# Optimization experiments

Measured on AMD Instinct MI355X. Metric: run time of the kernel, lower is better.

Reference implementation:

```python
import jax, jax.numpy as jnp
import numpy as np

EMBED = 1024
HEADS = 16
HEAD_DIM = EMBED // HEADS
LN_EPS = 1e-5


def _layer_norm(x, g, b):
    m = jnp.mean(x, axis=-1, keepdims=True)
    v = jnp.mean((x - m) ** 2, axis=-1, keepdims=True)
    return (x - m) / jnp.sqrt(v + LN_EPS) * g + b


def _rope(x):
    # x: (b, H, n, D); standard rotary: freqs repeated (cat(freqs, freqs)), rotate_half
    D = x.shape[-1]
    n = x.shape[2]
    inv_freq = 1.0 / (10000.0 ** (jnp.arange(0, D, 2, dtype=jnp.float32) / D))
    freqs = jnp.arange(n, dtype=jnp.float32)[:, None] * inv_freq[None, :]  # (n, D/2)
    emb = jnp.concatenate([freqs, freqs], axis=-1)  # (n, D)
    cos, sin = jnp.cos(emb), jnp.sin(emb)
    rot = jnp.concatenate([-x[..., D // 2:], x[..., : D // 2]], axis=-1)
    return x * cos + rot * sin


def setup_inputs() -> dict:
    key = jax.random.key(0)
    ks = jax.random.split(key, 8)
    E = EMBED
    s_in = 1.0 / np.sqrt(E)
    return {
        "x": jax.random.normal(ks[0], (2, 2048, E), dtype=jnp.float32),
        "in_proj_w": jax.random.uniform(ks[1], (3 * E, E), jnp.float32, -s_in, s_in),
        "in_proj_b": jnp.zeros((3 * E,), jnp.float32),
        "out_proj_w": jax.random.uniform(ks[2], (E, E), jnp.float32, -s_in, s_in),
        "out_proj_b": jnp.zeros((E,), jnp.float32),
        "geglu_w": jax.random.uniform(ks[3], (2 * E, E), jnp.float32, -s_in, s_in),
        "geglu_b": jnp.zeros((2 * E,), jnp.float32),
        "ln1_g": jnp.ones((E,), jnp.float32),
        "ln1_b": jnp.zeros((E,), jnp.float32),
        "ln2_g": jnp.ones((E,), jnp.float32),
        "ln2_b": jnp.zeros((E,), jnp.float32),
    }


def reference(x, in_proj_w, in_proj_b, out_proj_w, out_proj_b,
              geglu_w, geglu_b, ln1_g, ln1_b, ln2_g, ln2_b):
    b, n, E = x.shape
    H, D = HEADS, HEAD_DIM

    # RoPE applied to raw x (q = k = v = x in the module)
    xh = x.reshape(b, n, H, D).transpose(0, 2, 1, 3)  # (b,H,n,D)
    qr = _rope(xh)
    kr = qr  # q and k are identical pre-projection
    q = qr.transpose(0, 2, 1, 3).reshape(b, n, E)
    k = kr.transpose(0, 2, 1, 3).reshape(b, n, E)
    v = x

    # MultiheadAttention (batch-first semantics): in-proj, per-head SDPA, out-proj
    w_q, w_k, w_v = jnp.split(in_proj_w, 3, axis=0)
    b_q, b_k, b_v = jnp.split(in_proj_b, 3, axis=0)
    qp = (q @ w_q.T + b_q).reshape(b, n, H, D).transpose(0, 2, 1, 3)
    kp = (k @ w_k.T + b_k).reshape(b, n, H, D).transpose(0, 2, 1, 3)
    vp = (v @ w_v.T + b_v).reshape(b, n, H, D).transpose(0, 2, 1, 3)
    scores = jnp.einsum("bhqd,bhkd->bhqk", qp, kp) / jnp.sqrt(jnp.float32(D))
    attn = jax.nn.softmax(scores, axis=-1)
    ctx = jnp.einsum("bhqk,bhkd->bhqd", attn, vp)
    ctx = ctx.transpose(0, 2, 1, 3).reshape(b, n, E)
    attn_out = ctx @ out_proj_w.T + out_proj_b

    # residual + LN1
    h = _layer_norm(x + attn_out, ln1_g, ln1_b)

    # GeGLU: Linear(E -> 2E), chunk, value * gelu(gate) (exact erf gelu like torch)
    proj = h @ geglu_w.T + geglu_b
    val, gate = jnp.split(proj, 2, axis=-1)
    fc_out = val * jax.nn.gelu(gate, approximate=False)

    # residual + LN2
    return _layer_norm(h + fc_out, ln2_g, ln2_b)
```

## Files before the change

kernel.cpp:

```cpp
#include <hip/hip_runtime.h>


typedef __bf16 bf16;
typedef bf16 bf16x8 __attribute__((ext_vector_type(8)));
typedef bf16 bf16x4 __attribute__((ext_vector_type(4)));
typedef float f32x4 __attribute__((ext_vector_type(4)));
typedef float f32x16 __attribute__((ext_vector_type(16)));

#define EMB 1024
#define SEQ 2048
#define NTOK 4096
#define NH 16
#define HD 64

__device__ __forceinline__ f32x4 mfma16(bf16x8 a, bf16x8 b, f32x4 c) {
  return __builtin_amdgcn_mfma_f32_16x16x32_bf16(a, b, c, 0, 0, 0);
}
__device__ __forceinline__ f32x16 mfma32(bf16x8 a, bf16x8 b, f32x16 c) {
  return __builtin_amdgcn_mfma_f32_32x32x16_bf16(a, b, c, 0, 0, 0);
}

__device__ __forceinline__ void gll16(const void* g, void* l) {
  __builtin_amdgcn_global_load_lds(
      (const __attribute__((address_space(1))) void*)g,
      (__attribute__((address_space(3))) void*)l, 16, 0, 0);
}

__device__ __forceinline__ unsigned pk2(float a, float b) {
  union { bf16 h[2]; unsigned u; } t;
  t.h[0] = (bf16)a; t.h[1] = (bf16)b;
  return t.u;
}


__global__ __launch_bounds__(256) void rope_cast(
    const float* __restrict__ x, bf16* __restrict__ xb, bf16* __restrict__ qr) {
  int idx = blockIdx.x * 256 + threadIdx.x;
  int row = idx >> 9;
  int i = idx & 511;
  int h = i >> 5, d2 = i & 31;
  int pos = row & (SEQ - 1);
  int c0 = h * HD + d2;
  size_t base = (size_t)row * EMB;
  float x0 = x[base + c0], x1 = x[base + c0 + 32];
  float invf = exp2f(-(float)d2 * 0.4152410118609203f);
  float ang = (float)pos * invf;
  float sn, cs;
  sincosf(ang, &sn, &cs);
  qr[base + c0] = (bf16)(x0 * cs - x1 * sn);
  qr[base + c0 + 32] = (bf16)(x1 * cs + x0 * sn);
  xb[base + c0] = (bf16)x0;
  xb[base + c0 + 32] = (bf16)x1;
}

__global__ __launch_bounds__(256) void cast_w(
    const float* __restrict__ w, bf16* __restrict__ o, int n) {
  int i = (blockIdx.x * 256 + threadIdx.x) * 4;
  if (i < n) {
    float4 f = *(const float4*)(w + i);
    o[i] = (bf16)f.x; o[i + 1] = (bf16)f.y;
    o[i + 2] = (bf16)f.z; o[i + 3] = (bf16)f.w;
  }
}

__global__ __launch_bounds__(256) void gemm_in(
    const bf16* __restrict__ Aq, const bf16* __restrict__ Ax,
    const bf16* __restrict__ W, const float* __restrict__ bias,
    bf16* __restrict__ qk, bf16* __restrict__ vT) {
  __shared__ bf16 As[128 * 32];
  __shared__ bf16 Bs[128 * 32];
  const int tid = threadIdx.x, lane = tid & 63, wave = tid >> 6;
  const int quad = lane >> 4, l16 = lane & 15;
  const int m0 = blockIdx.y * 128, n0 = blockIdx.x * 128;
  const bf16* A = (n0 < 2048) ? Aq : Ax;
  const int K = 1024;
  const int wm = (wave >> 1) * 64, wn = (wave & 1) * 64;
  const int srow = wave * 32 + (lane >> 2);
  const int scol = (lane & 3) * 8;
  f32x4 acc[4][4] = {};
  for (int k0 = 0; k0 < K; k0 += 32) {
    __syncthreads();
    gll16(A + (size_t)(m0 + srow) * K + k0 + scol, As + wave * 1024);
    gll16(A + (size_t)(m0 + srow + 16) * K + k0 + scol, As + wave * 1024 + 512);
    gll16(W + (size_t)(n0 + srow) * K + k0 + scol, Bs + wave * 1024);
    gll16(W + (size_t)(n0 + srow + 16) * K + k0 + scol, Bs + wave * 1024 + 512);
    __syncthreads();
    bf16x8 af[4], bw[4];
#pragma unroll
    for (int t = 0; t < 4; ++t) {
      af[t] = *(const bf16x8*)(As + (wm + t * 16 + l16) * 32 + quad * 8);
      bw[t] = *(const bf16x8*)(Bs + (wn + t * 16 + l16) * 32 + quad * 8);
    }
#pragma unroll
    for (int mt = 0; mt < 4; ++mt)
#pragma unroll
      for (int nt = 0; nt < 4; ++nt)
        acc[mt][nt] = mfma16(af[mt], bw[nt], acc[mt][nt]);
  }
  if (n0 < 2048) {
#pragma unroll
    for (int mt = 0; mt < 4; ++mt)
      for (int nt = 0; nt < 4; ++nt) {
        const int n = n0 + wn + nt * 16 + l16;
        const float bv = bias[n];
#pragma unroll
        for (int r = 0; r < 4; ++r) {
          const int m = m0 + wm + mt * 16 + quad * 4 + r;
          qk[(size_t)m * 2048 + n] = (bf16)(acc[mt][nt][r] + bv);
        }
      }
  } else {
#pragma unroll
    for (int mt = 0; mt < 4; ++mt)
      for (int nt = 0; nt < 4; ++nt) {
        const int n = n0 + wn + nt * 16 + l16;
        const float bv = bias[n];
        const int m = m0 + wm + mt * 16 + quad * 4;
        const int bb = m >> 11, s = m & 2047;
        bf16x4 pkv;
#pragma unroll
        for (int r = 0; r < 4; ++r) pkv[r] = (bf16)(acc[mt][nt][r] + bv);
        *(bf16x4*)(vT + (((size_t)bb * 1024 + (n - 2048)) << 11) + s) = pkv;
      }
  }
}

__global__ __launch_bounds__(256) void gemm_bt(
    const bf16* __restrict__ A, const bf16* __restrict__ W,
    const float* __restrict__ bias,
    float* __restrict__ outF, bf16* __restrict__ outB,
    int M, int N, int K) {
  __shared__ bf16 As[128 * 32];
  __shared__ bf16 Bs[128 * 32];
  const int tid = threadIdx.x, lane = tid & 63, wave = tid >> 6;
  const int quad = lane >> 4, l16 = lane & 15;
  const int m0 = blockIdx.y * 128, n0 = blockIdx.x * 128;
  const int wm = (wave >> 1) * 64, wn = (wave & 1) * 64;
  const int srow = wave * 32 + (lane >> 2);
  const int scol = (lane & 3) * 8;
  f32x4 acc[4][4] = {};
  for (int k0 = 0; k0 < K; k0 += 32) {
    __syncthreads();
    gll16(A + (size_t)(m0 + srow) * K + k0 + scol, As + wave * 1024);
    gll16(A + (size_t)(m0 + srow + 16) * K + k0 + scol, As + wave * 1024 + 512);
    gll16(W + (size_t)(n0 + srow) * K + k0 + scol, Bs + wave * 1024);
    gll16(W + (size_t)(n0 + srow + 16) * K + k0 + scol, Bs + wave * 1024 + 512);
    __syncthreads();
    bf16x8 af[4], bw[4];
#pragma unroll
    for (int t = 0; t < 4; ++t) {
      af[t] = *(const bf16x8*)(As + (wm + t * 16 + l16) * 32 + quad * 8);
      bw[t] = *(const bf16x8*)(Bs + (wn + t * 16 + l16) * 32 + quad * 8);
    }
#pragma unroll
    for (int mt = 0; mt < 4; ++mt)
#pragma unroll
      for (int nt = 0; nt < 4; ++nt)
        acc[mt][nt] = mfma16(af[mt], bw[nt], acc[mt][nt]);
  }
#pragma unroll
  for (int mt = 0; mt < 4; ++mt)
    for (int nt = 0; nt < 4; ++nt) {
      const int n = n0 + wn + nt * 16 + l16;
      const float bv = bias ? bias[n] : 0.0f;
#pragma unroll
      for (int r = 0; r < 4; ++r) {
        const int m = m0 + wm + mt * 16 + quad * 4 + r;
        const float v = acc[mt][nt][r] + bv;
        if (outF) outF[(size_t)m * N + n] = v;
        if (outB) outB[(size_t)m * N + n] = (bf16)v;
      }
    }
}

__global__ __launch_bounds__(256) void gemm_bt64(
    const bf16* __restrict__ A, const bf16* __restrict__ W,
    const float* __restrict__ bias, float* __restrict__ outF,
    int M, int N, int K) {
  __shared__ bf16 As[128 * 32];
  __shared__ bf16 Bs[64 * 32];
  const int tid = threadIdx.x, lane = tid & 63, wave = tid >> 6;
  const int quad = lane >> 4, l16 = lane & 15;
  const int m0 = blockIdx.y * 128, n0 = blockIdx.x * 64;
  const int wm = (wave >> 1) * 64, wn = (wave & 1) * 32;
  const int srow = wave * 32 + (lane >> 2);
  const int srowB = wave * 16 + (lane >> 2);
  const int scol = (lane & 3) * 8;
  f32x4 acc[4][2] = {};
  for (int k0 = 0; k0 < K; k0 += 32) {
    __syncthreads();
    gll16(A + (size_t)(m0 + srow) * K + k0 + scol, As + wave * 1024);
    gll16(A + (size_t)(m0 + srow + 16) * K + k0 + scol, As + wave * 1024 + 512);
    gll16(W + (size_t)(n0 + srowB) * K + k0 + scol, Bs + wave * 512);
    __syncthreads();
    bf16x8 af[4], bw[2];
#pragma unroll
    for (int t = 0; t < 4; ++t)
      af[t] = *(const bf16x8*)(As + (wm + t * 16 + l16) * 32 + quad * 8);
#pragma unroll
    for (int t = 0; t < 2; ++t)
      bw[t] = *(const bf16x8*)(Bs + (wn + t * 16 + l16) * 32 + quad * 8);
#pragma unroll
    for (int mt = 0; mt < 4; ++mt)
#pragma unroll
      for (int nt = 0; nt < 2; ++nt)
        acc[mt][nt] = mfma16(af[mt], bw[nt], acc[mt][nt]);
  }
#pragma unroll
  for (int mt = 0; mt < 4; ++mt)
    for (int nt = 0; nt < 2; ++nt) {
      const int n = n0 + wn + nt * 16 + l16;
      const float bv = bias[n];
#pragma unroll
      for (int r = 0; r < 4; ++r) {
        const int m = m0 + wm + mt * 16 + quad * 4 + r;
        outF[(size_t)m * N + n] = acc[mt][nt][r] + bv;
      }
    }
}

__global__ __launch_bounds__(256) void attn7(
    const bf16* __restrict__ QK, const bf16* __restrict__ VT,
    bf16* __restrict__ ctx) {
  __shared__ __align__(16) bf16 Ks[2][64 * 64];
  __shared__ __align__(16) bf16 Vs[2][64 * 64];
  __shared__ float Linv[4][32];
  const int tid = threadIdx.x, lane = tid & 63, wave = tid >> 6;
  const int hi = lane >> 5, l31 = lane & 31, l7 = lane & 7;
  const int bid = blockIdx.x;
  const int hb = (bid & 7) * 4 + ((bid >> 3) & 3);
  const int qt = bid >> 5;
  const int h = hb & 15, b = hb >> 4;

  bf16x8 qf[4];
  {
    const int qrow = qt * 128 + wave * 32 + l31;
    const bf16* qp = QK + (size_t)(b * SEQ + qrow) * 2048 + h * HD + hi * 8;
#pragma unroll
    for (int t = 0; t < 4; ++t) {
      bf16x8 v = *(const bf16x8*)(qp + t * 16);
#pragma unroll
      for (int j = 0; j < 8; ++j) v[j] = (bf16)((float)v[j] * 0.125f);
      qf[t] = v;
    }
  }
  f32x16 o0 = {}, o1 = {};
  float lpart = 0.0f;

  const int srow = tid >> 3;
  const int sc16 = tid & 7;
  const bf16* kg = QK + (size_t)(b * SEQ) * 2048 + 1024 + h * HD + sc16 * 8;
  const bf16* vg = VT + ((size_t)(b * NH + h) * HD) * 2048 + sc16 * 8;
  const int g4lo = 2 * sc16 - (sc16 & 1);

  bf16x8 kcur[2], vcur[2];
#pragma unroll
  for (int p = 0; p < 2; ++p) {
    const int row = p * 32 + srow;
    kcur[p] = *(const bf16x8*)(kg + (size_t)row * 2048);
    vcur[p] = *(const bf16x8*)(vg + (size_t)row * 2048);
  }
#pragma unroll
  for (int p = 0; p < 2; ++p) {
    const int row = p * 32 + srow;
    const int m2 = (row & 7) << 1;
    *(bf16x8*)(Ks[0] + row * 64 + ((sc16 ^ (row & 7)) * 8)) = kcur[p];
    union { bf16x8 v; unsigned long long q[2]; } u2;
    u2.v = vcur[p];
    *(unsigned long long*)(Vs[0] + row * 64 + ((g4lo ^ m2) * 4)) = u2.q[0];
    *(unsigned long long*)(Vs[0] + row * 64 + (((g4lo + 2) ^ m2) * 4)) = u2.q[1];
  }
#pragma unroll
  for (int p = 0; p < 2; ++p) {
    const int row = p * 32 + srow;
    kcur[p] = *(const bf16x8*)(kg + (size_t)(64 + row) * 2048);
    vcur[p] = *(const bf16x8*)(vg + (size_t)row * 2048 + 64);
  }

  for (int t = 0; t < 32; ++t) {
    __syncthreads();
    const bf16* ks = Ks[t & 1];
    const bf16* vs = Vs[t & 1];
    if (t + 1 < 32) {
      bf16* kd = Ks[(t + 1) & 1];
      bf16* vd = Vs[(t + 1) & 1];
#pragma unroll
      for (int p = 0; p < 2; ++p) {
        const int row = p * 32 + srow;
        const int m2 = (row & 7) << 1;
        *(bf16x8*)(kd + row * 64 + ((sc16 ^ (row & 7)) * 8)) = kcur[p];
        union { bf16x8 v; unsigned long long q[2]; } u2;
        u2.v = vcur[p];
        *(unsigned long long*)(vd + row * 64 + ((g4lo ^ m2) * 4)) = u2.q[0];
        *(unsigned long long*)(vd + row * 64 + (((g4lo + 2) ^ m2) * 4)) = u2.q[1];
      }
      if (t + 2 < 32) {
        const int kb2 = (t + 2) * 64;
#pragma unroll
        for (int p = 0; p < 2; ++p) {
          const int row = p * 32 + srow;
          kcur[p] = *(const bf16x8*)(kg + (size_t)(kb2 + row) * 2048);
          vcur[p] = *(const bf16x8*)(vg + (size_t)row * 2048 + kb2);
        }
      }
    }
    f32x16 s0 = {}, s1 = {};
#pragma unroll
    for (int tt = 0; tt < 4; ++tt) {
      const int swc = ((tt * 2 + hi) ^ l7) * 8;
      bf16x8 k0 = *(const bf16x8*)(ks + l31 * 64 + swc);
      bf16x8 k1 = *(const bf16x8*)(ks + (32 + l31) * 64 + swc);
      s0 = mfma32(k0, qf[tt], s0);
      s1 = mfma32(k1, qf[tt], s1);
    }
    unsigned u[16];
#pragma unroll
    for (int g = 0; g < 8; ++g) {
      const int base = (g & 3) * 4;
      float e0, e1, e2, e3;
      if (g < 4) {
        e0 = __expf(s0[base]); e1 = __expf(s0[base + 1]);
        e2 = __expf(s0[base + 2]); e3 = __expf(s0[base + 3]);
      } else {
        e0 = __expf(s1[base]); e1 = __expf(s1[base + 1]);
        e2 = __expf(s1[base + 2]); e3 = __expf(s1[base + 3]);
      }
      lpart += (e0 + e1) + (e2 + e3);
      u[g * 2] = pk2(e0, e1);
      u[g * 2 + 1] = pk2(e2, e3);
    }
#pragma unroll
    for (int kk = 0; kk < 4; ++kk) {
      union { unsigned w[4]; bf16x8 v; } fw;
      fw.w[0] = u[4 * kk]; fw.w[1] = u[4 * kk + 1];
      fw.w[2] = u[4 * kk + 2]; fw.w[3] = u[4 * kk + 3];
      const int swz = (4 * kk + 2 * hi) ^ (l7 << 1);
      bf16x8 v0 = *(const bf16x8*)(vs + l31 * 64 + swz * 4);
      bf16x8 v1 = *(const bf16x8*)(vs + (32 + l31) * 64 + swz * 4);
      o0 = mfma32(fw.v, v0, o0);
      o1 = mfma32(fw.v, v1, o1);
    }
  }
  float ltot = lpart + __shfl_xor(lpart, 32, 64);
  if (lane < 32) Linv[wave][lane] = 1.0f / ltot;
#pragma unroll
  for (int r = 0; r < 16; ++r) {
    const int qloc = (r & 3) + 8 * (r >> 2) + 4 * hi;
    const float inv = Linv[wave][qloc];
    const int qrow = qt * 128 + wave * 32 + qloc;
    bf16* cp = ctx + (size_t)(b * SEQ + qrow) * EMB + h * HD;
    cp[l31] = (bf16)(o0[r] * inv);
    cp[32 + l31] = (bf16)(o1[r] * inv);
  }
}

__global__ __launch_bounds__(256) void ln1_k(
    const float* __restrict__ x, const float* __restrict__ ao,
    const float* __restrict__ g, const float* __restrict__ bta,
    float* __restrict__ hF, bf16* __restrict__ hB) {
  int row = blockIdx.x, tid = threadIdx.x;
  const float* xr = x + (size_t)row * EMB;
  const float* ar = ao + (size_t)row * EMB;
  float v[4], s = 0.0f, s2 = 0.0f;
#pragma unroll
  for (int i = 0; i < 4; ++i) {
    float t = xr[tid + i * 256] + ar[tid + i * 256];
    v[i] = t; s += t; s2 += t * t;
  }
#pragma unroll
  for (int off = 1; off < 64; off <<= 1) {
    s += __shfl_xor(s, off, 64);
    s2 += __shfl_xor(s2, off, 64);
  }
  __shared__ float red[8];
  int wave = tid >> 6, lane = tid & 63;
  if (lane == 0) { red[wave] = s; red[4 + wave] = s2; }
  __syncthreads();
  s = red[0] + red[1] + red[2] + red[3];
  s2 = red[4] + red[5] + red[6] + red[7];
  float mean = s * (1.0f / EMB);
  float var = s2 * (1.0f / EMB) - mean * mean;
  float inv = rsqrtf(var + 1e-5f);
#pragma unroll
  for (int i = 0; i < 4; ++i) {
    int c = tid + i * 256;
    float t = (v[i] - mean) * inv * g[c] + bta[c];
    hF[(size_t)row * EMB + c] = t;
    hB[(size_t)row * EMB + c] = (bf16)t;
  }
}

__global__ __launch_bounds__(256) void geglu_ln2(
    const float* __restrict__ h, const bf16* __restrict__ proj,
    const float* __restrict__ g, const float* __restrict__ bta,
    float* __restrict__ out) {
  int row = blockIdx.x, tid = threadIdx.x;
  const float* hr = h + (size_t)row * EMB;
  const bf16* pr = proj + (size_t)row * 2048;
  float v[4], s = 0.0f, s2 = 0.0f;
#pragma unroll
  for (int i = 0; i < 4; ++i) {
    int c = tid + i * 256;
    float val = (float)pr[c];
    float gate = (float)pr[1024 + c];
    float ge = 0.5f * gate * (1.0f + erff(gate * 0.70710678f));
    float t = hr[c] + val * ge;
    v[i] = t; s += t; s2 += t * t;
  }
#pragma unroll
  for (int off = 1; off < 64; off <<= 1) {
    s += __shfl_xor(s, off, 64);
    s2 += __shfl_xor(s2, off, 64);
  }
  __shared__ float red[8];
  int wave = tid >> 6, lane = tid & 63;
  if (lane == 0) { red[wave] = s; red[4 + wave] = s2; }
  __syncthreads();
  s = red[0] + red[1] + red[2] + red[3];
  s2 = red[4] + red[5] + red[6] + red[7];
  float mean = s * (1.0f / EMB);
  float var = s2 * (1.0f / EMB) - mean * mean;
  float inv = rsqrtf(var + 1e-5f);
#pragma unroll
  for (int i = 0; i < 4; ++i) {
    int c = tid + i * 256;
    out[(size_t)row * EMB + c] = (v[i] - mean) * inv * g[c] + bta[c];
  }
}

extern "C" void kernel_launch(void* const* d_in, const int* in_sizes, int n_in,
                              void* d_out, int out_size, void* d_ws, size_t ws_size,
                              hipStream_t stream) {
  const float* x = (const float*)d_in[0];
  const float* inW = (const float*)d_in[1];
  const float* inB = (const float*)d_in[2];
  const float* outW = (const float*)d_in[3];
  const float* opB = (const float*)d_in[4];
  const float* ggW = (const float*)d_in[5];
  const float* ggB = (const float*)d_in[6];
  const float* g1 = (const float*)d_in[7];
  const float* b1 = (const float*)d_in[8];
  const float* g2 = (const float*)d_in[9];
  const float* b2 = (const float*)d_in[10];
  float* out = (float*)d_out;
  char* ws = (char*)d_ws;
  const size_t MB = 1ull << 20;
  bf16* xb = (bf16*)(ws);
  bf16* qr = (bf16*)(ws + 8 * MB);
  bf16* ctx = (bf16*)(ws + 8 * MB);
  bf16* wI = (bf16*)(ws + 16 * MB);
  bf16* wO = (bf16*)(ws + 22 * MB);
  bf16* wG = (bf16*)(ws + 24 * MB);
  bf16* qk = (bf16*)(ws + 28 * MB);
  bf16* projB = (bf16*)(ws + 28 * MB);
  bf16* vbT = (bf16*)(ws + 44 * MB);
  float* ao = (float*)(ws + 44 * MB);
  bf16* hB = (bf16*)(ws + 60 * MB);

  rope_cast<<<NTOK * 512 / 256, 256, 0, stream>>>(x, xb, qr);
  cast_w<<<(3072 * 1024 / 4) / 256, 256, 0, stream>>>(inW, wI, 3072 * 1024);
  cast_w<<<(1024 * 1024 / 4) / 256, 256, 0, stream>>>(outW, wO, 1024 * 1024);
  cast_w<<<(2048 * 1024 / 4) / 256, 256, 0, stream>>>(ggW, wG, 2048 * 1024);
  gemm_in<<<dim3(24, 32), 256, 0, stream>>>(qr, xb, wI, inB, qk, vbT);
  attn7<<<512, 256, 0, stream>>>(qk, vbT, ctx);
  gemm_bt64<<<dim3(16, 32), 256, 0, stream>>>(ctx, wO, opB, ao,
                                              NTOK, 1024, 1024);
  ln1_k<<<NTOK, 256, 0, stream>>>(x, ao, g1, b1, ao, hB);
  gemm_bt<<<dim3(16, 32), 256, 0, stream>>>(hB, wG, ggB, nullptr, projB,
                                            NTOK, 2048, 1024);
  geglu_ln2<<<NTOK, 256, 0, stream>>>(ao, projB, g2, b2, out);
}
```

Before: 273.8 us.

## Split attention keys across wave pairs and reduce partial outputs in LDS

The attention kernel now gives each block 64 query rows instead of 128, and each pair of waves splits every 64-key tile into two halves. Partial outputs and softmax denominators are combined through shared memory at the end, and the launch grid doubles to 1024 blocks. The V tile staging also changes to two 8-byte global loads per row followed by a single 16-byte swizzled LDS store. The aim is more parallelism and occupancy on the attention stage, at the cost of loading each K/V tile for half as many queries and adding an extra reduction and barriers.

New measurement: 282.0 us. 3.0% more time.

```diff
diff --git a/kernel.cpp b/kernel.cpp
--- a/kernel.cpp
+++ b/kernel.cpp
@@ -219,14 +219,15 @@
     }
 }
 
-__global__ __launch_bounds__(256) void attn7(
+__global__ __launch_bounds__(256) void attn8(
     const bf16* __restrict__ QK, const bf16* __restrict__ VT,
     bf16* __restrict__ ctx) {
-  __shared__ __align__(16) bf16 Ks[2][64 * 64];
-  __shared__ __align__(16) bf16 Vs[2][64 * 64];
-  __shared__ float Linv[4][32];
+  __shared__ __align__(16) bf16 Ks[2][4096];
+  __shared__ __align__(16) bf16 Vs[2][4096];
+  __shared__ float Linv2[2][32];
   const int tid = threadIdx.x, lane = tid & 63, wave = tid >> 6;
   const int hi = lane >> 5, l31 = lane & 31, l7 = lane & 7;
+  const int qgrp = wave & 1, khalf = wave >> 1;
   const int bid = blockIdx.x;
   const int hb = (bid & 7) * 4 + ((bid >> 3) & 3);
   const int qt = bid >> 5;
@@ -234,7 +235,7 @@
 
   bf16x8 qf[4];
   {
-    const int qrow = qt * 128 + wave * 32 + l31;
+    const int qrow = qt * 64 + qgrp * 32 + l31;
     const bf16* qp = QK + (size_t)(b * SEQ + qrow) * 2048 + h * HD + hi * 8;
 #pragma unroll
     for (int t = 0; t < 4; ++t) {
@@ -249,32 +250,35 @@
 
   const int srow = tid >> 3;
   const int sc16 = tid & 7;
+  const int tq = sc16 >> 1;
+  const int og = tq * 16 + (sc16 & 1) * 4;
   const bf16* kg = QK + (size_t)(b * SEQ) * 2048 + 1024 + h * HD + sc16 * 8;
-  const bf16* vg = VT + ((size_t)(b * NH + h) * HD) * 2048 + sc16 * 8;
-  const int g4lo = 2 * sc16 - (sc16 & 1);
-
-  bf16x8 kcur[2], vcur[2];
+  const bf16* vgr = VT + ((size_t)(b * NH + h) * HD) * 2048;
+
+  bf16x8 kcur[2];
+  uint2 va[2], vb[2];
 #pragma unroll
   for (int p = 0; p < 2; ++p) {
     const int row = p * 32 + srow;
     kcur[p] = *(const bf16x8*)(kg + (size_t)row * 2048);
-    vcur[p] = *(const bf16x8*)(vg + (size_t)row * 2048);
+    va[p] = *(const uint2*)(vgr + (size_t)row * 2048 + og);
+    vb[p] = *(const uint2*)(vgr + (size_t)row * 2048 + og + 8);
   }
 #pragma unroll
   for (int p = 0; p < 2; ++p) {
     const int row = p * 32 + srow;
-    const int m2 = (row & 7) << 1;
-    *(bf16x8*)(Ks[0] + row * 64 + ((sc16 ^ (row & 7)) * 8)) = kcur[p];
-    union { bf16x8 v; unsigned long long q[2]; } u2;
-    u2.v = vcur[p];
-    *(unsigned long long*)(Vs[0] + row * 64 + ((g4lo ^ m2) * 4)) = u2.q[0];
-    *(unsigned long long*)(Vs[0] + row * 64 + (((g4lo + 2) ^ m2) * 4)) = u2.q[1];
+    const int sw = row * 64 + ((sc16 ^ (row & 7)) * 8);
+    *(bf16x8*)(Ks[0] + sw) = kcur[p];
+    union { uint2 u2[2]; bf16x8 v; } vv;
+    vv.u2[0] = va[p]; vv.u2[1] = vb[p];
+    *(bf16x8*)(Vs[0] + sw) = vv.v;
   }
 #pragma unroll
   for (int p = 0; p < 2; ++p) {
     const int row = p * 32 + srow;
     kcur[p] = *(const bf16x8*)(kg + (size_t)(64 + row) * 2048);
-    vcur[p] = *(const bf16x8*)(vg + (size_t)row * 2048 + 64);
+    va[p] = *(const uint2*)(vgr + (size_t)row * 2048 + 64 + og);
+    vb[p] = *(const uint2*)(vgr + (size_t)row * 2048 + 64 + og + 8);
   }
 
   for (int t = 0; t < 32; ++t) {
@@ -287,12 +291,11 @@
 #pragma unroll
       for (int p = 0; p < 2; ++p) {
         const int row = p * 32 + srow;
-        const int m2 = (row & 7) << 1;
-        *(bf16x8*)(kd + row * 64 + ((sc16 ^ (row & 7)) * 8)) = kcur[p];
-        union { bf16x8 v; unsigned long long q[2]; } u2;
-        u2.v = vcur[p];
-        *(unsigned long long*)(vd + row * 64 + ((g4lo ^ m2) * 4)) = u2.q[0];
-        *(unsigned long long*)(vd + row * 64 + (((g4lo + 2) ^ m2) * 4)) = u2.q[1];
+        const int sw = row * 64 + ((sc16 ^ (row & 7)) * 8);
+        *(bf16x8*)(kd + sw) = kcur[p];
+        union { uint2 u2[2]; bf16x8 v; } vv;
+        vv.u2[0] = va[p]; vv.u2[1] = vb[p];
+        *(bf16x8*)(vd + sw) = vv.v;
       }
       if (t + 2 < 32) {
         const int kb2 = (t + 2) * 64;
@@ -300,40 +303,35 @@
         for (int p = 0; p < 2; ++p) {
           const int row = p * 32 + srow;
           kcur[p] = *(const bf16x8*)(kg + (size_t)(kb2 + row) * 2048);
-          vcur[p] = *(const bf16x8*)(vg + (size_t)row * 2048 + kb2);
+          va[p] = *(const uint2*)(vgr + (size_t)row * 2048 + kb2 + og);
+          vb[p] = *(const uint2*)(vgr + (size_t)row * 2048 + kb2 + og + 8);
         }
       }
     }
-    f32x16 s0 = {}, s1 = {};
+    f32x16 s0 = {};
 #pragma unroll
     for (int tt = 0; tt < 4; ++tt) {
-      const int swc = ((tt * 2 + hi) ^ l7) * 8;
-      bf16x8 k0 = *(const bf16x8*)(ks + l31 * 64 + swc);
-      bf16x8 k1 = *(const bf16x8*)(ks + (32 + l31) * 64 + swc);
-      s0 = mfma32(k0, qf[tt], s0);
-      s1 = mfma32(k1, qf[tt], s1);
-    }
-    unsigned u[16];
-#pragma unroll
-    for (int g = 0; g < 8; ++g) {
-      const int base = (g & 3) * 4;
-      float e0, e1, e2, e3;
-      if (g < 4) {
-        e0 = __expf(s0[base]); e1 = __expf(s0[base + 1]);
-        e2 = __expf(s0[base + 2]); e3 = __expf(s0[base + 3]);
-      } else {
-        e0 = __expf(s1[base]); e1 = __expf(s1[base + 1]);
-        e2 = __expf(s1[base + 2]); e3 = __expf(s1[base + 3]);
-      }
+      bf16x8 kf = *(const bf16x8*)(
+          ks + (khalf * 32 + l31) * 64 + (((tt * 2 + hi) ^ l7) * 8));
+      s0 = mfma32(kf, qf[tt], s0);
+    }
+    unsigned u[8];
+#pragma unroll
+    for (int g = 0; g < 4; ++g) {
+      float e0 = __expf(s0[g * 4]);
+      float e1 = __expf(s0[g * 4 + 1]);
+      float e2 = __expf(s0[g * 4 + 2]);
+      float e3 = __expf(s0[g * 4 + 3]);
       lpart += (e0 + e1) + (e2 + e3);
       u[g * 2] = pk2(e0, e1);
       u[g * 2 + 1] = pk2(e2, e3);
     }
 #pragma unroll
-    for (int kk = 0; kk < 4; ++kk) {
+    for (int kl = 0; kl < 2; ++kl) {
+      const int kk = 2 * khalf + kl;
       union { unsigned w[4]; bf16x8 v; } fw;
-      fw.w[0] = u[4 * kk]; fw.w[1] = u[4 * kk + 1];
-      fw.w[2] = u[4 * kk + 2]; fw.w[3] = u[4 * kk + 3];
+      fw.w[0] = u[4 * kl]; fw.w[1] = u[4 * kl + 1];
+      fw.w[2] = u[4 * kl + 2]; fw.w[3] = u[4 * kl + 3];
       const int swz = (4 * kk + 2 * hi) ^ (l7 << 1);
       bf16x8 v0 = *(const bf16x8*)(vs + l31 * 64 + swz * 4);
       bf16x8 v1 = *(const bf16x8*)(vs + (32 + l31) * 64 + swz * 4);
@@ -341,16 +339,45 @@
       o1 = mfma32(fw.v, v1, o1);
     }
   }
-  float ltot = lpart + __shfl_xor(lpart, 32, 64);
-  if (lane < 32) Linv[wave][lane] = 1.0f / ltot;
-#pragma unroll
-  for (int r = 0; r < 16; ++r) {
-    const int qloc = (r & 3) + 8 * (r >> 2) + 4 * hi;
-    const float inv = Linv[wave][qloc];
-    const int qrow = qt * 128 + wave * 32 + qloc;
-    bf16* cp = ctx + (size_t)(b * SEQ + qrow) * EMB + h * HD;
-    cp[l31] = (bf16)(o0[r] * inv);
-    cp[32 + l31] = (bf16)(o1[r] * inv);
+  __syncthreads();
+  float* Osh = (float*)Ks;
+  float* Lsh = (float*)Vs;
+  if (khalf) {
+    float* ob = Osh + qgrp * 2048;
+#pragma unroll
+    for (int c = 0; c < 4; ++c) {
+      f32x4 t0 = {o0[4 * c], o0[4 * c + 1], o0[4 * c + 2], o0[4 * c + 3]};
+      f32x4 t1 = {o1[4 * c], o1[4 * c + 1], o1[4 * c + 2], o1[4 * c + 3]};
+      *(f32x4*)(ob + c * 256 + lane * 4) = t0;
+      *(f32x4*)(ob + 1024 + c * 256 + lane * 4) = t1;
+    }
+    Lsh[qgrp * 64 + lane] = lpart;
+  }
+  __syncthreads();
+  if (!khalf) {
+    float* ob = Osh + qgrp * 2048;
+#pragma unroll
+    for (int c = 0; c < 4; ++c) {
+      f32x4 t0 = *(const f32x4*)(ob + c * 256 + lane * 4);
+      f32x4 t1 = *(const f32x4*)(ob + 1024 + c * 256 + lane * 4);
+#pragma unroll
+      for (int j = 0; j < 4; ++j) {
+        o0[4 * c + j] += t0[j];
+        o1[4 * c + j] += t1[j];
+      }
+    }
+    lpart += Lsh[qgrp * 64 + lane];
+    float ltot = lpart + __shfl_xor(lpart, 32, 64);
+    if (lane < 32) Linv2[qgrp][lane] = 1.0f / ltot;
+#pragma unroll
+    for (int r = 0; r < 16; ++r) {
+      const int qloc = (r & 3) + 8 * (r >> 2) + 4 * hi;
+      const float inv = Linv2[qgrp][qloc];
+      const int qrow = qt * 64 + qgrp * 32 + qloc;
+      bf16* cp = ctx + (size_t)(b * SEQ + qrow) * EMB + h * HD;
+      cp[l31] = (bf16)(o0[r] * inv);
+      cp[32 + l31] = (bf16)(o1[r] * inv);
+    }
   }
 }
 
@@ -462,7 +489,7 @@
   cast_w<<<(1024 * 1024 / 4) / 256, 256, 0, stream>>>(outW, wO, 1024 * 1024);
   cast_w<<<(2048 * 1024 / 4) / 256, 256, 0, stream>>>(ggW, wG, 2048 * 1024);
   gemm_in<<<dim3(24, 32), 256, 0, stream>>>(qr, xb, wI, inB, qk, vbT);
-  attn7<<<512, 256, 0, stream>>>(qk, vbT, ctx);
+  attn8<<<1024, 256, 0, stream>>>(qk, vbT, ctx);
   gemm_bt64<<<dim3(16, 32), 256, 0, stream>>>(ctx, wO, opB, ao,
                                               NTOK, 1024, 1024);
   ln1_k<<<NTOK, 256, 0, stream>>>(x, ao, g1, b1, ao, hB);
```

## Double attention KV tile to 128 keys per stage with new V layout

Applied to the files above, without the earlier changes.

The attention kernel now stages 128 keys per iteration instead of 64, halving the number of loop iterations and block-wide barriers. The V tile moves to a 128-column swizzled LDS layout loaded with paired 8-byte global reads, and each stage runs two 64-key halves of the QK/softmax/PV compute. Shared memory per block doubles to about 64 KB and more prefetch registers are held, which may reduce occupancy.

Result: no change. 272.5 us (-0.5%).

```diff
diff --git a/kernel.cpp b/kernel.cpp
--- a/kernel.cpp
+++ b/kernel.cpp
@@ -219,11 +219,11 @@
     }
 }
 
-__global__ __launch_bounds__(256) void attn7(
+__global__ __launch_bounds__(256) void attn9(
     const bf16* __restrict__ QK, const bf16* __restrict__ VT,
     bf16* __restrict__ ctx) {
-  __shared__ __align__(16) bf16 Ks[2][64 * 64];
-  __shared__ __align__(16) bf16 Vs[2][64 * 64];
+  __shared__ __align__(16) bf16 Ks[2][8192];
+  __shared__ __align__(16) bf16 Vs[2][8192];
   __shared__ float Linv[4][32];
   const int tid = threadIdx.x, lane = tid & 63, wave = tid >> 6;
   const int hi = lane >> 5, l31 = lane & 31, l7 = lane & 7;
@@ -247,98 +247,103 @@
   f32x16 o0 = {}, o1 = {};
   float lpart = 0.0f;
 
-  const int srow = tid >> 3;
-  const int sc16 = tid & 7;
-  const bf16* kg = QK + (size_t)(b * SEQ) * 2048 + 1024 + h * HD + sc16 * 8;
-  const bf16* vg = VT + ((size_t)(b * NH + h) * HD) * 2048 + sc16 * 8;
-  const int g4lo = 2 * sc16 - (sc16 & 1);
-
-  bf16x8 kcur[2], vcur[2];
-#pragma unroll
-  for (int p = 0; p < 2; ++p) {
-    const int row = p * 32 + srow;
-    kcur[p] = *(const bf16x8*)(kg + (size_t)row * 2048);
-    vcur[p] = *(const bf16x8*)(vg + (size_t)row * 2048);
-  }
-#pragma unroll
-  for (int p = 0; p < 2; ++p) {
-    const int row = p * 32 + srow;
-    const int m2 = (row & 7) << 1;
-    *(bf16x8*)(Ks[0] + row * 64 + ((sc16 ^ (row & 7)) * 8)) = kcur[p];
-    union { bf16x8 v; unsigned long long q[2]; } u2;
-    u2.v = vcur[p];
-    *(unsigned long long*)(Vs[0] + row * 64 + ((g4lo ^ m2) * 4)) = u2.q[0];
-    *(unsigned long long*)(Vs[0] + row * 64 + (((g4lo + 2) ^ m2) * 4)) = u2.q[1];
-  }
-#pragma unroll
-  for (int p = 0; p < 2; ++p) {
-    const int row = p * 32 + srow;
-    kcur[p] = *(const bf16x8*)(kg + (size_t)(64 + row) * 2048);
-    vcur[p] = *(const bf16x8*)(vg + (size_t)row * 2048 + 64);
-  }
-
-  for (int t = 0; t < 32; ++t) {
+  const int krow0 = tid >> 3;
+  const int ksc = tid & 7;
+  const int vrow0 = tid >> 4;
+  const int vc16 = tid & 15;
+  const int og = (vc16 >> 1) * 16 + (vc16 & 1) * 4;
+  const bf16* kg = QK + (size_t)(b * SEQ) * 2048 + 1024 + h * HD + ksc * 8;
+  const bf16* vg = VT + ((size_t)(b * NH + h) * HD) * 2048;
+
+  bf16x8 kcur[4];
+  uint2 va[4], vb[4];
+#pragma unroll
+  for (int p = 0; p < 4; ++p) {
+    kcur[p] = *(const bf16x8*)(kg + (size_t)(krow0 + p * 32) * 2048);
+    va[p] = *(const uint2*)(vg + (size_t)(vrow0 + p * 16) * 2048 + og);
+    vb[p] = *(const uint2*)(vg + (size_t)(vrow0 + p * 16) * 2048 + og + 8);
+  }
+#pragma unroll
+  for (int p = 0; p < 4; ++p) {
+    const int kr = krow0 + p * 32;
+    *(bf16x8*)(Ks[0] + kr * 64 + ((ksc ^ (kr & 7)) * 8)) = kcur[p];
+    const int vr = vrow0 + p * 16;
+    union { uint2 u2[2]; bf16x8 v; } vv;
+    vv.u2[0] = va[p]; vv.u2[1] = vb[p];
+    *(bf16x8*)(Vs[0] + vr * 128 + ((vc16 ^ (vr & 7)) * 8)) = vv.v;
+  }
+#pragma unroll
+  for (int p = 0; p < 4; ++p) {
+    kcur[p] = *(const bf16x8*)(kg + (size_t)(128 + krow0 + p * 32) * 2048);
+    va[p] = *(const uint2*)(vg + (size_t)(vrow0 + p * 16) * 2048 + 128 + og);
+    vb[p] = *(const uint2*)(vg + (size_t)(vrow0 + p * 16) * 2048 + 128 + og + 8);
+  }
+
+  for (int t = 0; t < 16; ++t) {
     __syncthreads();
     const bf16* ks = Ks[t & 1];
     const bf16* vs = Vs[t & 1];
-    if (t + 1 < 32) {
+    if (t + 1 < 16) {
       bf16* kd = Ks[(t + 1) & 1];
       bf16* vd = Vs[(t + 1) & 1];
 #pragma unroll
-      for (int p = 0; p < 2; ++p) {
-        const int row = p * 32 + srow;
-        const int m2 = (row & 7) << 1;
-        *(bf16x8*)(kd + row * 64 + ((sc16 ^ (row & 7)) * 8)) = kcur[p];
-        union { bf16x8 v; unsigned long long q[2]; } u2;
-        u2.v = vcur[p];
-        *(unsigned long long*)(vd + row * 64 + ((g4lo ^ m2) * 4)) = u2.q[0];
-        *(unsigned long long*)(vd + row * 64 + (((g4lo + 2) ^ m2) * 4)) = u2.q[1];
-      }
-      if (t + 2 < 32) {
-        const int kb2 = (t + 2) * 64;
-#pragma unroll
-        for (int p = 0; p < 2; ++p) {
-          const int row = p * 32 + srow;
-          kcur[p] = *(const bf16x8*)(kg + (size_t)(kb2 + row) * 2048);
-          vcur[p] = *(const bf16x8*)(vg + (size_t)row * 2048 + kb2);
+      for (int p = 0; p < 4; ++p) {
+        const int kr = krow0 + p * 32;
+        *(bf16x8*)(kd + kr * 64 + ((ksc ^ (kr & 7)) * 8)) = kcur[p];
+        const int vr = vrow0 + p * 16;
+        union { uint2 u2[2]; bf16x8 v; } vv;
+        vv.u2[0] = va[p]; vv.u2[1] = vb[p];
+        *(bf16x8*)(vd + vr * 128 + ((vc16 ^ (vr & 7)) * 8)) = vv.v;
+      }
+      if (t + 2 < 16) {
+        const int kb2 = (t + 2) * 128;
+#pragma unroll
+        for (int p = 0; p < 4; ++p) {
+          kcur[p] = *(const bf16x8*)(kg + (size_t)(kb2 + krow0 + p * 32) * 2048);
+          va[p] = *(const uint2*)(vg + (size_t)(vrow0 + p * 16) * 2048 + kb2 + og);
+          vb[p] = *(const uint2*)(vg + (size_t)(vrow0 + p * 16) * 2048 + kb2 + og + 8);
         }
       }
     }
-    f32x16 s0 = {}, s1 = {};
-#pragma unroll
-    for (int tt = 0; tt < 4; ++tt) {
-      const int swc = ((tt * 2 + hi) ^ l7) * 8;
-      bf16x8 k0 = *(const bf16x8*)(ks + l31 * 64 + swc);
-      bf16x8 k1 = *(const bf16x8*)(ks + (32 + l31) * 64 + swc);
-      s0 = mfma32(k0, qf[tt], s0);
-      s1 = mfma32(k1, qf[tt], s1);
-    }
-    unsigned u[16];
-#pragma unroll
-    for (int g = 0; g < 8; ++g) {
-      const int base = (g & 3) * 4;
-      float e0, e1, e2, e3;
-      if (g < 4) {
-        e0 = __expf(s0[base]); e1 = __expf(s0[base + 1]);
-        e2 = __expf(s0[base + 2]); e3 = __expf(s0[base + 3]);
-      } else {
-        e0 = __expf(s1[base]); e1 = __expf(s1[base + 1]);
-        e2 = __expf(s1[base + 2]); e3 = __expf(s1[base + 3]);
-      }
-      lpart += (e0 + e1) + (e2 + e3);
-      u[g * 2] = pk2(e0, e1);
-      u[g * 2 + 1] = pk2(e2, e3);
-    }
-#pragma unroll
-    for (int kk = 0; kk < 4; ++kk) {
-      union { unsigned w[4]; bf16x8 v; } fw;
-      fw.w[0] = u[4 * kk]; fw.w[1] = u[4 * kk + 1];
-      fw.w[2] = u[4 * kk + 2]; fw.w[3] = u[4 * kk + 3];
-      const int swz = (4 * kk + 2 * hi) ^ (l7 << 1);
-      bf16x8 v0 = *(const bf16x8*)(vs + l31 * 64 + swz * 4);
-      bf16x8 v1 = *(const bf16x8*)(vs + (32 + l31) * 64 + swz * 4);
-      o0 = mfma32(fw.v, v0, o0);
-      o1 = mfma32(fw.v, v1, o1);
+#pragma unroll
+    for (int half = 0; half < 2; ++half) {
+      const bf16* ksh = ks + half * 64 * 64;
+      f32x16 s0 = {}, s1 = {};
+#pragma unroll
+      for (int tt = 0; tt < 4; ++tt) {
+        const int swc = ((tt * 2 + hi) ^ l7) * 8;
+        bf16x8 k0 = *(const bf16x8*)(ksh + l31 * 64 + swc);
+        bf16x8 k1 = *(const bf16x8*)(ksh + (32 + l31) * 64 + swc);
+        s0 = mfma32(k0, qf[tt], s0);
+        s1 = mfma32(k1, qf[tt], s1);
+      }
+      unsigned u[16];
+#pragma unroll
+      for (int g = 0; g < 8; ++g) {
+        const int base = (g & 3) * 4;
+        float e0, e1, e2, e3;
+        if (g < 4) {
+          e0 = __expf(s0[base]); e1 = __expf(s0[base + 1]);
+          e2 = __expf(s0[base + 2]); e3 = __expf(s0[base + 3]);
+        } else {
+          e0 = __expf(s1[base]); e1 = __expf(s1[base + 1]);
+          e2 = __expf(s1[base + 2]); e3 = __expf(s1[base + 3]);
+        }
+        lpart += (e0 + e1) + (e2 + e3);
+        u[g * 2] = pk2(e0, e1);
+        u[g * 2 + 1] = pk2(e2, e3);
+      }
+#pragma unroll
+      for (int kk = 0; kk < 4; ++kk) {
+        union { unsigned w[4]; bf16x8 v; } fw;
+        fw.w[0] = u[4 * kk]; fw.w[1] = u[4 * kk + 1];
+        fw.w[2] = u[4 * kk + 2]; fw.w[3] = u[4 * kk + 3];
+        const int c16 = (8 * half + 2 * kk + hi) ^ l7;
+        bf16x8 v0 = *(const bf16x8*)(vs + l31 * 128 + c16 * 8);
+        bf16x8 v1 = *(const bf16x8*)(vs + (32 + l31) * 128 + c16 * 8);
+        o0 = mfma32(fw.v, v0, o0);
+        o1 = mfma32(fw.v, v1, o1);
+      }
     }
   }
   float ltot = lpart + __shfl_xor(lpart, 32, 64);
@@ -462,7 +467,7 @@
   cast_w<<<(1024 * 1024 / 4) / 256, 256, 0, stream>>>(outW, wO, 1024 * 1024);
   cast_w<<<(2048 * 1024 / 4) / 256, 256, 0, stream>>>(ggW, wG, 2048 * 1024);
   gemm_in<<<dim3(24, 32), 256, 0, stream>>>(qr, xb, wI, inB, qk, vbT);
-  attn7<<<512, 256, 0, stream>>>(qk, vbT, ctx);
+  attn9<<<512, 256, 0, stream>>>(qk, vbT, ctx);
   gemm_bt64<<<dim3(16, 32), 256, 0, stream>>>(ctx, wO, opB, ao,
                                               NTOK, 1024, 1024);
   ln1_k<<<NTOK, 256, 0, stream>>>(x, ao, g1, b1, ao, hB);
```
